# Performance work log

Hardware: AMD Instinct MI355X
Metric: run time of the kernel (lower is better)

## Reference

```python
import jax, jax.numpy as jnp
import numpy as np

N, M, E = 50000, 50000, 1600000
D_IN, HID, OUT = 128, 128, 128


def setup_inputs() -> dict:
    key = jax.random.key(0)
    ks = jax.random.split(key, 8)
    query = jax.random.normal(ks[0], (N, D_IN), jnp.float32)
    memory = jax.random.normal(ks[1], (M, D_IN), jnp.float32)
    adj_vals = jnp.ones((E,), jnp.float32)  # tf.sparse adjacency values (typically 1.0)
    Wq = jax.random.normal(ks[2], (D_IN, HID), jnp.float32) * 0.05
    bq = jnp.zeros((HID,), jnp.float32)
    Wk = jax.random.normal(ks[3], (D_IN, HID), jnp.float32) * 0.05
    bk = jnp.zeros((HID,), jnp.float32)
    Wv = jax.random.normal(ks[4], (D_IN, OUT), jnp.float32) * 0.05
    bv = jnp.zeros((OUT,), jnp.float32)
    rows = jnp.sort(jax.random.randint(ks[5], (E,), 0, N, jnp.int32))
    cols = jax.random.randint(ks[6], (E,), 0, M, jnp.int32)
    return {"query": query, "memory": memory, "adj_vals": adj_vals,
            "Wq": Wq, "bq": bq, "Wk": Wk, "bk": bk, "Wv": Wv, "bv": bv,
            "rows": rows, "cols": cols}


def reference(query, memory, adj_vals, Wq, bq, Wk, bk, Wv, bv, rows, cols):
    n = query.shape[0]
    hid = Wq.shape[1]
    # Dense projections with gelu (tfa.activations.gelu default approximate=True)
    q = jax.nn.gelu(query @ Wq + bq, approximate=True)   # [n, hid]
    k = jax.nn.gelu(memory @ Wk + bk, approximate=True)  # [m, hid]
    v = jax.nn.gelu(memory @ Wv + bv, approximate=True)  # [m, out]
    # Edge-level scores = (q_i . k_j) / sqrt(hid) * adj_val  (== coef * adj_matrix)
    scores = jnp.sum(q[rows] * k[cols], axis=-1)          # [E]
    scores = scores * (adj_vals / jnp.sqrt(jnp.float32(hid)))
    # Sparse softmax over nonzero entries of each row (tf.sparse.softmax)
    row_max = jax.ops.segment_max(scores, rows, num_segments=n, indices_are_sorted=True)
    row_max = jnp.where(jnp.isfinite(row_max), row_max, 0.0)  # rows with no edges
    e = jnp.exp(scores - row_max[rows])
    denom = jax.ops.segment_sum(e, rows, num_segments=n, indices_are_sorted=True)
    w = e / denom[rows]                                   # [E]
    # Sparse-dense matmul: out_i = sum_j w_ij * v_j
    out = jax.ops.segment_sum(w[:, None] * v[cols], rows, num_segments=n, indices_are_sorted=True)
    return out
```

## Files before the change

### kernel.cpp

```cpp
#include <hip/hip_runtime.h>
#include <hip/hip_bf16.h>
#include <hip/hip_fp8.h>
#include <math.h>

typedef _Float16 f16x4 __attribute__((ext_vector_type(4)));
typedef _Float16 f16x8 __attribute__((ext_vector_type(8)));
typedef float f32x4 __attribute__((ext_vector_type(4)));
typedef __fp16 hf8 __attribute__((ext_vector_type(8)));

#define DIM 128
#define LDST 136

#if defined(__has_builtin)
#if __has_builtin(__builtin_amdgcn_cvt_pk_fp8_f32) && __has_builtin(__builtin_amdgcn_cvt_pk_f32_fp8)
#define HAVE_FP8CVT 1
#endif
#endif

__device__ __forceinline__ unsigned int pack_fp8x4(float f0, float f1, float f2, float f3) {
#ifdef HAVE_FP8CVT
    int w = __builtin_amdgcn_cvt_pk_fp8_f32(f0, f1, 0, false);
    w = __builtin_amdgcn_cvt_pk_fp8_f32(f2, f3, w, true);
    return (unsigned int)w;
#else
    __hip_fp8_e4m3 a(f0), b(f1), c(f2), d(f3);
    return (unsigned int)a.__x | ((unsigned int)b.__x << 8) |
           ((unsigned int)c.__x << 16) | ((unsigned int)d.__x << 24);
#endif
}

__device__ __forceinline__ void dot_fp8x4(float& d, unsigned int w, const float* qv) {
#ifdef HAVE_FP8CVT
    auto lo = __builtin_amdgcn_cvt_pk_f32_fp8((int)w, false);
    auto hi = __builtin_amdgcn_cvt_pk_f32_fp8((int)w, true);
    d += lo[0] * qv[0] + lo[1] * qv[1] + hi[0] * qv[2] + hi[1] * qv[3];
#else
    for (int j = 0; j < 4; ++j) {
        __hip_fp8_e4m3 t; t.__x = (unsigned char)((w >> (8 * j)) & 0xff);
        d += (float)t * qv[j];
    }
#endif
}

__global__ __launch_bounds__(256) void prep_w_kernel(
    const float* __restrict__ Wq, const float* __restrict__ Wk,
    const float* __restrict__ Wv, _Float16* __restrict__ Wt)
{
    const float* W = (blockIdx.y == 0) ? Wq : (blockIdx.y == 1) ? Wk : Wv;
    _Float16* dst = Wt + (size_t)blockIdx.y * DIM * DIM;
    int idx = blockIdx.x * 256 + threadIdx.x;
    int k = idx >> 7;
    int n = idx & 127;
    dst[n * DIM + k] = (_Float16)W[idx];
}

__global__ __launch_bounds__(256) void row_ptr_kernel(
    const int* __restrict__ rows, int* __restrict__ row_ptr, int n, int e)
{
    int r = blockIdx.x * 256 + threadIdx.x;
    if (r > n) return;
    if (r == n) { row_ptr[n] = e; return; }
    int lo = 0, hi = e;
    while (lo < hi) {
        int mid = (lo + hi) >> 1;
        if (rows[mid] < r) lo = mid + 1; else hi = mid;
    }
    row_ptr[r] = lo;
}

__global__ __launch_bounds__(256, 2) void proj_gemm_kernel(
    const float* __restrict__ query, const float* __restrict__ memory,
    const _Float16* __restrict__ Wt,
    const float* __restrict__ bq, const float* __restrict__ bk,
    const float* __restrict__ bv,
    _Float16* __restrict__ qf, unsigned char* __restrict__ k8,
    _Float16* __restrict__ v16, int n, int m)
{
    __shared__ _Float16 xs[128 * LDST];

    int which = blockIdx.y;
    const float* X    = (which == 0) ? query : memory;
    const _Float16* Wm = Wt + (size_t)which * DIM * DIM;
    const float* bias = (which == 0) ? bq : (which == 1) ? bk : bv;
    int R             = (which == 0) ? n : m;

    int tid = threadIdx.x;
    int rowblock = blockIdx.x * 128;
    if (rowblock >= R) return;

    for (int it = 0; it < 16; ++it) {
        int flat = it * 256 + tid;
        int r  = flat >> 5;
        int c4 = (flat & 31) * 4;
        int gr = rowblock + r;
        if (gr >= R) gr = R - 1;
        float4 x = *(const float4*)(X + (size_t)gr * DIM + c4);
        f16x4 w4;
        w4[0] = (_Float16)x.x; w4[1] = (_Float16)x.y;
        w4[2] = (_Float16)x.z; w4[3] = (_Float16)x.w;
        *(f16x4*)(&xs[r * LDST + c4]) = w4;
    }
    __syncthreads();

    int wave = tid >> 6;
    int lane = tid & 63;
    int quad = lane >> 4;
    int l16  = lane & 15;
    int wrow = wave * 32;

    f16x8 afrag[2][4];
    for (int rt = 0; rt < 2; ++rt)
        for (int ks = 0; ks < 4; ++ks)
            afrag[rt][ks] = *(const f16x8*)(&xs[(wrow + rt * 16 + l16) * LDST + quad * 8 + ks * 32]);

    f32x4 acc[8][2];
    for (int ct = 0; ct < 8; ++ct) { acc[ct][0] = {0,0,0,0}; acc[ct][1] = {0,0,0,0}; }
    for (int ct = 0; ct < 8; ++ct) {
        const _Float16* wp = Wm + (size_t)(ct * 16 + l16) * DIM + quad * 8;
        for (int ks = 0; ks < 4; ++ks) {
            f16x8 b = *(const f16x8*)(wp + ks * 32);
            acc[ct][0] = __builtin_amdgcn_mfma_f32_16x16x32_f16(afrag[0][ks], b, acc[ct][0], 0, 0, 0);
            acc[ct][1] = __builtin_amdgcn_mfma_f32_16x16x32_f16(afrag[1][ks], b, acc[ct][1], 0, 0, 0);
        }
    }

    __syncthreads();
    for (int ct = 0; ct < 8; ++ct) {
        float bval = bias[ct * 16 + l16];
        for (int rt = 0; rt < 2; ++rt) {
            for (int reg = 0; reg < 4; ++reg) {
                float x = acc[ct][rt][reg] + bval;
                float t  = 0.7978845608028654f * (x + 0.044715f * x * x * x);
                float th = 1.0f - 2.0f / (__expf(2.0f * t) + 1.0f);
                float g  = 0.5f * x * (1.0f + th);
                xs[(wrow + rt * 16 + quad * 4 + reg) * LDST + ct * 16 + l16] = (_Float16)g;
            }
        }
    }
    __syncthreads();

    if (which == 1) {
        for (int it = 0; it < 8; ++it) {
            int flat = it * 256 + tid;
            int r  = flat >> 4;
            int c8 = (flat & 15) * 8;
            int gr = rowblock + r;
            if (gr < R) {
                f16x8 h = *(const f16x8*)(&xs[r * LDST + c8]);
                unsigned int w0 = pack_fp8x4((float)h[0], (float)h[1], (float)h[2], (float)h[3]);
                unsigned int w1 = pack_fp8x4((float)h[4], (float)h[5], (float)h[6], (float)h[7]);
                *(uint2*)(k8 + (size_t)gr * DIM + c8) = make_uint2(w0, w1);
            }
        }
    } else {
        _Float16* Ybase = (which == 0) ? qf : v16;
        for (int it = 0; it < 8; ++it) {
            int flat = it * 256 + tid;
            int r  = flat >> 4;
            int c8 = (flat & 15) * 8;
            int gr = rowblock + r;
            if (gr < R) {
                f16x8 vv = *(const f16x8*)(&xs[r * LDST + c8]);
                *(f16x8*)(Ybase + (size_t)gr * DIM + c8) = vv;
            }
        }
    }
}

__global__ __launch_bounds__(256) void edge_attn_kernel(
    const __fp16* __restrict__ qf, const unsigned char* __restrict__ k8,
    const __fp16* __restrict__ v16, const float* __restrict__ adj_vals,
    const int* __restrict__ cols, const int* __restrict__ row_ptr,
    float* __restrict__ out, int n)
{
    int row = blockIdx.x * 4 + (threadIdx.x >> 6);
    if (row >= n) return;
    int lane    = threadIdx.x & 63;
    int quarter = lane >> 4;
    int l16     = lane & 15;

    int start = row_ptr[row];
    int end   = row_ptr[row + 1];

    float qv[8];
    {
        hf8 q8 = *(const hf8*)(qf + (size_t)row * DIM + l16 * 8);
#pragma unroll
        for (int j = 0; j < 8; ++j) qv[j] = (float)q8[j];
    }

    float s_sum = 0.0f;
    float acc[8];
#pragma unroll
    for (int j = 0; j < 8; ++j) acc[j] = 0.0f;

    const float scale = 0.08838834764831845f;

    for (int g = start; g < end; g += 8) {
        int eA = g + quarter;
        int eB = g + 4 + quarter;
        bool vA = eA < end;
        bool vB = eB < end;
        int last = end - 1;
        int iA = vA ? eA : last;
        int iB = vB ? eB : last;
        int   cA = cols[iA];
        int   cB = cols[iB];
        float aA = adj_vals[iA] * scale;
        float aB = adj_vals[iB] * scale;

        uint2 rA = *(const uint2*)(k8 + (size_t)cA * DIM + l16 * 8);
        uint2 rB = *(const uint2*)(k8 + (size_t)cB * DIM + l16 * 8);
        hf8 vA8 = *(const hf8*)(v16 + (size_t)cA * DIM + l16 * 8);
        hf8 vB8 = *(const hf8*)(v16 + (size_t)cB * DIM + l16 * 8);

        float dA = 0.0f, dB = 0.0f;
        dot_fp8x4(dA, rA.x, qv);
        dot_fp8x4(dA, rA.y, qv + 4);
        dot_fp8x4(dB, rB.x, qv);
        dot_fp8x4(dB, rB.y, qv + 4);
        dA += __shfl_xor(dA, 1); dB += __shfl_xor(dB, 1);
        dA += __shfl_xor(dA, 2); dB += __shfl_xor(dB, 2);
        dA += __shfl_xor(dA, 4); dB += __shfl_xor(dB, 4);
        dA += __shfl_xor(dA, 8); dB += __shfl_xor(dB, 8);

        float pA_ = vA ? __expf(dA * aA) : 0.0f;
        float pB_ = vB ? __expf(dB * aB) : 0.0f;
        s_sum += pA_ + pB_;
#pragma unroll
        for (int j = 0; j < 8; ++j)
            acc[j] += pA_ * (float)vA8[j] + pB_ * (float)vB8[j];
    }

    s_sum += __shfl_xor(s_sum, 16);
    s_sum += __shfl_xor(s_sum, 32);
#pragma unroll
    for (int j = 0; j < 8; ++j) {
        acc[j] += __shfl_xor(acc[j], 16);
        acc[j] += __shfl_xor(acc[j], 32);
    }
    float inv = (s_sum > 0.0f) ? 1.0f / s_sum : 0.0f;

    if (quarter == 0) {
        float4* dst = (float4*)(out + (size_t)row * DIM + l16 * 8);
        dst[0] = make_float4(acc[0] * inv, acc[1] * inv, acc[2] * inv, acc[3] * inv);
        dst[1] = make_float4(acc[4] * inv, acc[5] * inv, acc[6] * inv, acc[7] * inv);
    }
}

extern "C" void kernel_launch(void* const* d_in, const int* in_sizes, int n_in,
                              void* d_out, int out_size, void* d_ws, size_t ws_size,
                              hipStream_t stream)
{
    const float* query    = (const float*)d_in[0];
    const float* memory   = (const float*)d_in[1];
    const float* adj_vals = (const float*)d_in[2];
    const float* Wq       = (const float*)d_in[3];
    const float* bq       = (const float*)d_in[4];
    const float* Wk       = (const float*)d_in[5];
    const float* bk       = (const float*)d_in[6];
    const float* Wv       = (const float*)d_in[7];
    const float* bv       = (const float*)d_in[8];
    const int*   rows     = (const int*)d_in[9];
    const int*   cols     = (const int*)d_in[10];
    float* out = (float*)d_out;

    int n = in_sizes[0] / DIM;
    int m = in_sizes[1] / DIM;
    int e = in_sizes[9];

    char* ws = (char*)d_ws;
    size_t off = 0;
    _Float16* Wt = (_Float16*)(ws + off); off += (size_t)3 * DIM * DIM * 2;
    _Float16* qf = (_Float16*)(ws + off); off += (size_t)n * DIM * 2;
    _Float16* v16 = (_Float16*)(ws + off); off += (size_t)m * DIM * 2;
    unsigned char* k8 = (unsigned char*)(ws + off); off += (size_t)m * DIM;
    int* row_ptr = (int*)(ws + off);      off += (size_t)(n + 1) * 4;

    prep_w_kernel<<<dim3(64, 3), 256, 0, stream>>>(Wq, Wk, Wv, Wt);

    row_ptr_kernel<<<dim3((n + 1 + 255) / 256), 256, 0, stream>>>(rows, row_ptr, n, e);

    proj_gemm_kernel<<<dim3((n + 127) / 128, 3), 256, 0, stream>>>(
        query, memory, Wt, bq, bk, bv, qf, k8, v16, n, m);

    edge_attn_kernel<<<dim3((n + 3) / 4), 256, 0, stream>>>(
        (const __fp16*)qf, k8, (const __fp16*)v16, adj_vals, cols, row_ptr, out, n);
}
```

Baseline: 236.4 us.

## Bucket edges by column range within each row and pack col/adj pairs

Adds a per-call counting sort that reorders each row's edges into 16 column buckets. Column indices and adjacency values are packed into one uint2 array, so the attention kernel does one load per edge instead of two. Edges whose columns fall in the same range are then processed closer together across rows, which should improve cache locality for the k8/v16 gathers. The cost is three extra kernels, a memset, global atomics, and an extra write and read of an E-sized buffer on every call. The attention scale is also folded into q once per row.

```diff
diff --git a/kernel.cpp b/kernel.cpp
--- a/kernel.cpp
+++ b/kernel.cpp
@@ -10,6 +10,7 @@
 
 #define DIM 128
 #define LDST 136
+#define NB 16
 
 #if defined(__has_builtin)
 #if __has_builtin(__builtin_amdgcn_cvt_pk_fp8_f32) && __has_builtin(__builtin_amdgcn_cvt_pk_f32_fp8)
@@ -66,6 +67,45 @@
         if (rows[mid] < r) lo = mid + 1; else hi = mid;
     }
     row_ptr[r] = lo;
+}
+
+__global__ __launch_bounds__(256) void count_kernel(
+    const int* __restrict__ rows, const int* __restrict__ cols,
+    int* __restrict__ cnt, int e, int bsize)
+{
+    int i = blockIdx.x * 256 + threadIdx.x;
+    if (i >= e) return;
+    int b = cols[i] / bsize;
+    atomicAdd(&cnt[rows[i] * NB + b], 1);
+}
+
+__global__ __launch_bounds__(256) void prefix_kernel(
+    const int* __restrict__ row_ptr, int* __restrict__ cnt, int n)
+{
+    int r = blockIdx.x * 256 + threadIdx.x;
+    if (r >= n) return;
+    int acc = row_ptr[r];
+    for (int b = 0; b < NB; ++b) {
+        int c = cnt[r * NB + b];
+        cnt[r * NB + b] = acc;
+        acc += c;
+    }
+}
+
+__global__ __launch_bounds__(256) void scatter_kernel(
+    const int* __restrict__ rows, const int* __restrict__ cols,
+    const float* __restrict__ adj, int* __restrict__ cnt,
+    uint2* __restrict__ packed, int e, int bsize)
+{
+    int i = blockIdx.x * 256 + threadIdx.x;
+    if (i >= e) return;
+    int c = cols[i];
+    int b = c / bsize;
+    int slot = atomicAdd(&cnt[rows[i] * NB + b], 1);
+    uint2 p;
+    p.x = (unsigned int)c;
+    p.y = __float_as_uint(adj[i]);
+    packed[slot] = p;
 }
 
 __global__ __launch_bounds__(256, 2) void proj_gemm_kernel(
@@ -169,9 +209,8 @@
 
 __global__ __launch_bounds__(256) void edge_attn_kernel(
     const __fp16* __restrict__ qf, const unsigned char* __restrict__ k8,
-    const __fp16* __restrict__ v16, const float* __restrict__ adj_vals,
-    const int* __restrict__ cols, const int* __restrict__ row_ptr,
-    float* __restrict__ out, int n)
+    const __fp16* __restrict__ v16, const uint2* __restrict__ packed,
+    const int* __restrict__ row_ptr, float* __restrict__ out, int n)
 {
     int row = blockIdx.x * 4 + (threadIdx.x >> 6);
     if (row >= n) return;
@@ -182,19 +221,18 @@
     int start = row_ptr[row];
     int end   = row_ptr[row + 1];
 
+    const float scale = 0.08838834764831845f;
     float qv[8];
     {
         hf8 q8 = *(const hf8*)(qf + (size_t)row * DIM + l16 * 8);
 #pragma unroll
-        for (int j = 0; j < 8; ++j) qv[j] = (float)q8[j];
+        for (int j = 0; j < 8; ++j) qv[j] = (float)q8[j] * scale;
     }
 
     float s_sum = 0.0f;
     float acc[8];
 #pragma unroll
     for (int j = 0; j < 8; ++j) acc[j] = 0.0f;
-
-    const float scale = 0.08838834764831845f;
 
     for (int g = start; g < end; g += 8) {
         int eA = g + quarter;
@@ -204,10 +242,12 @@
         int last = end - 1;
         int iA = vA ? eA : last;
         int iB = vB ? eB : last;
-        int   cA = cols[iA];
-        int   cB = cols[iB];
-        float aA = adj_vals[iA] * scale;
-        float aB = adj_vals[iB] * scale;
+        uint2 pkA = packed[iA];
+        uint2 pkB = packed[iB];
+        int   cA = (int)pkA.x;
+        int   cB = (int)pkB.x;
+        float aA = __uint_as_float(pkA.y);
+        float aB = __uint_as_float(pkB.y);
 
         uint2 rA = *(const uint2*)(k8 + (size_t)cA * DIM + l16 * 8);
         uint2 rB = *(const uint2*)(k8 + (size_t)cB * DIM + l16 * 8);
@@ -268,6 +308,7 @@
     int n = in_sizes[0] / DIM;
     int m = in_sizes[1] / DIM;
     int e = in_sizes[9];
+    int bsize = (m + NB - 1) / NB;
 
     char* ws = (char*)d_ws;
     size_t off = 0;
@@ -275,15 +316,23 @@
     _Float16* qf = (_Float16*)(ws + off); off += (size_t)n * DIM * 2;
     _Float16* v16 = (_Float16*)(ws + off); off += (size_t)m * DIM * 2;
     unsigned char* k8 = (unsigned char*)(ws + off); off += (size_t)m * DIM;
+    uint2* packed = (uint2*)(ws + off);   off += (size_t)e * 8;
     int* row_ptr = (int*)(ws + off);      off += (size_t)(n + 1) * 4;
+    off = (off + 15) & ~(size_t)15;
+    int* cnt = (int*)(ws + off);          off += (size_t)n * NB * 4;
 
     prep_w_kernel<<<dim3(64, 3), 256, 0, stream>>>(Wq, Wk, Wv, Wt);
 
     row_ptr_kernel<<<dim3((n + 1 + 255) / 256), 256, 0, stream>>>(rows, row_ptr, n, e);
+
+    hipMemsetAsync(cnt, 0, (size_t)n * NB * 4, stream);
+    count_kernel<<<dim3((e + 255) / 256), 256, 0, stream>>>(rows, cols, cnt, e, bsize);
+    prefix_kernel<<<dim3((n + 255) / 256), 256, 0, stream>>>(row_ptr, cnt, n);
+    scatter_kernel<<<dim3((e + 255) / 256), 256, 0, stream>>>(rows, cols, adj_vals, cnt, packed, e, bsize);
 
     proj_gemm_kernel<<<dim3((n + 127) / 128, 3), 256, 0, stream>>>(
         query, memory, Wt, bq, bk, bv, qf, k8, v16, n, m);
 
     edge_attn_kernel<<<dim3((n + 3) / 4), 256, 0, stream>>>(
-        (const __fp16*)qf, k8, (const __fp16*)v16, adj_vals, cols, row_ptr, out, n);
-}
+        (const __fp16*)qf, k8, (const __fp16*)v16, packed, row_ptr, out, n);
+}
```

Measured after the change: 304.4 us. +28.8%, slower.

## Interleave fp8 K and fp16 V into one per-node record for edge gathers

Applied to the files above, without the earlier changes.

The projection kernel now writes each memory node's fp8 key row and fp16 value row into a single 384-byte record. The separate k8 and v16 buffers are gone. Each edge gather in the attention kernel therefore reads one contiguous region instead of two distant buffers, which is meant to improve DRAM and cache locality of the random column gathers. It also folds the 1/sqrt(hid) scale into q once per row and adds nontemporal hints on the streamed cols/adj_vals loads and the output stores. The risk is that the record layout changes little if gathers are already cache-line bound, and the nontemporal hints could hurt reuse.

```diff
diff --git a/kernel.cpp b/kernel.cpp
--- a/kernel.cpp
+++ b/kernel.cpp
@@ -10,6 +10,7 @@
 
 #define DIM 128
 #define LDST 136
+#define KVREC 384
 
 #if defined(__has_builtin)
 #if __has_builtin(__builtin_amdgcn_cvt_pk_fp8_f32) && __has_builtin(__builtin_amdgcn_cvt_pk_f32_fp8)
@@ -73,8 +74,8 @@
     const _Float16* __restrict__ Wt,
     const float* __restrict__ bq, const float* __restrict__ bk,
     const float* __restrict__ bv,
-    _Float16* __restrict__ qf, unsigned char* __restrict__ k8,
-    _Float16* __restrict__ v16, int n, int m)
+    _Float16* __restrict__ qf, unsigned char* __restrict__ kvrec,
+    int n, int m)
 {
     __shared__ _Float16 xs[128 * LDST];
 
@@ -149,11 +150,10 @@
                 f16x8 h = *(const f16x8*)(&xs[r * LDST + c8]);
                 unsigned int w0 = pack_fp8x4((float)h[0], (float)h[1], (float)h[2], (float)h[3]);
                 unsigned int w1 = pack_fp8x4((float)h[4], (float)h[5], (float)h[6], (float)h[7]);
-                *(uint2*)(k8 + (size_t)gr * DIM + c8) = make_uint2(w0, w1);
+                *(uint2*)(kvrec + (size_t)gr * KVREC + c8) = make_uint2(w0, w1);
             }
         }
-    } else {
-        _Float16* Ybase = (which == 0) ? qf : v16;
+    } else if (which == 2) {
         for (int it = 0; it < 8; ++it) {
             int flat = it * 256 + tid;
             int r  = flat >> 4;
@@ -161,17 +161,27 @@
             int gr = rowblock + r;
             if (gr < R) {
                 f16x8 vv = *(const f16x8*)(&xs[r * LDST + c8]);
-                *(f16x8*)(Ybase + (size_t)gr * DIM + c8) = vv;
+                *(f16x8*)(kvrec + (size_t)gr * KVREC + 128 + c8 * 2) = vv;
             }
         }
+    } else {
+        for (int it = 0; it < 8; ++it) {
+            int flat = it * 256 + tid;
+            int r  = flat >> 4;
+            int c8 = (flat & 15) * 8;
+            int gr = rowblock + r;
+            if (gr < R) {
+                f16x8 vv = *(const f16x8*)(&xs[r * LDST + c8]);
+                *(f16x8*)(qf + (size_t)gr * DIM + c8) = vv;
+            }
+        }
     }
 }
 
 __global__ __launch_bounds__(256) void edge_attn_kernel(
-    const __fp16* __restrict__ qf, const unsigned char* __restrict__ k8,
-    const __fp16* __restrict__ v16, const float* __restrict__ adj_vals,
-    const int* __restrict__ cols, const int* __restrict__ row_ptr,
-    float* __restrict__ out, int n)
+    const __fp16* __restrict__ qf, const unsigned char* __restrict__ kvrec,
+    const float* __restrict__ adj_vals, const int* __restrict__ cols,
+    const int* __restrict__ row_ptr, float* __restrict__ out, int n)
 {
     int row = blockIdx.x * 4 + (threadIdx.x >> 6);
     if (row >= n) return;
@@ -182,19 +192,18 @@
     int start = row_ptr[row];
     int end   = row_ptr[row + 1];
 
+    const float scale = 0.08838834764831845f;
     float qv[8];
     {
-        hf8 q8 = *(const hf8*)(qf + (size_t)row * DIM + l16 * 8);
+        hf8 q8 = __builtin_nontemporal_load((const hf8*)(qf + (size_t)row * DIM + l16 * 8));
 #pragma unroll
-        for (int j = 0; j < 8; ++j) qv[j] = (float)q8[j];
+        for (int j = 0; j < 8; ++j) qv[j] = (float)q8[j] * scale;
     }
 
     float s_sum = 0.0f;
     float acc[8];
 #pragma unroll
     for (int j = 0; j < 8; ++j) acc[j] = 0.0f;
-
-    const float scale = 0.08838834764831845f;
 
     for (int g = start; g < end; g += 8) {
         int eA = g + quarter;
@@ -204,15 +213,17 @@
         int last = end - 1;
         int iA = vA ? eA : last;
         int iB = vB ? eB : last;
-        int   cA = cols[iA];
-        int   cB = cols[iB];
-        float aA = adj_vals[iA] * scale;
-        float aB = adj_vals[iB] * scale;
-
-        uint2 rA = *(const uint2*)(k8 + (size_t)cA * DIM + l16 * 8);
-        uint2 rB = *(const uint2*)(k8 + (size_t)cB * DIM + l16 * 8);
-        hf8 vA8 = *(const hf8*)(v16 + (size_t)cA * DIM + l16 * 8);
-        hf8 vB8 = *(const hf8*)(v16 + (size_t)cB * DIM + l16 * 8);
+        int   cA = __builtin_nontemporal_load(cols + iA);
+        int   cB = __builtin_nontemporal_load(cols + iB);
+        float aA = __builtin_nontemporal_load(adj_vals + iA);
+        float aB = __builtin_nontemporal_load(adj_vals + iB);
+
+        const unsigned char* rAp = kvrec + (size_t)cA * KVREC;
+        const unsigned char* rBp = kvrec + (size_t)cB * KVREC;
+        uint2 rA = *(const uint2*)(rAp + l16 * 8);
+        uint2 rB = *(const uint2*)(rBp + l16 * 8);
+        hf8 vA8 = *(const hf8*)(rAp + 128 + l16 * 16);
+        hf8 vB8 = *(const hf8*)(rBp + 128 + l16 * 16);
 
         float dA = 0.0f, dB = 0.0f;
         dot_fp8x4(dA, rA.x, qv);
@@ -242,9 +253,11 @@
     float inv = (s_sum > 0.0f) ? 1.0f / s_sum : 0.0f;
 
     if (quarter == 0) {
-        float4* dst = (float4*)(out + (size_t)row * DIM + l16 * 8);
-        dst[0] = make_float4(acc[0] * inv, acc[1] * inv, acc[2] * inv, acc[3] * inv);
-        dst[1] = make_float4(acc[4] * inv, acc[5] * inv, acc[6] * inv, acc[7] * inv);
+        float* dst = out + (size_t)row * DIM + l16 * 8;
+        f32x4 o0 = {acc[0] * inv, acc[1] * inv, acc[2] * inv, acc[3] * inv};
+        f32x4 o1 = {acc[4] * inv, acc[5] * inv, acc[6] * inv, acc[7] * inv};
+        __builtin_nontemporal_store(o0, (f32x4*)dst);
+        __builtin_nontemporal_store(o1, (f32x4*)(dst + 4));
     }
 }
 
@@ -273,8 +286,7 @@
     size_t off = 0;
     _Float16* Wt = (_Float16*)(ws + off); off += (size_t)3 * DIM * DIM * 2;
     _Float16* qf = (_Float16*)(ws + off); off += (size_t)n * DIM * 2;
-    _Float16* v16 = (_Float16*)(ws + off); off += (size_t)m * DIM * 2;
-    unsigned char* k8 = (unsigned char*)(ws + off); off += (size_t)m * DIM;
+    unsigned char* kvrec = (unsigned char*)(ws + off); off += (size_t)m * KVREC;
     int* row_ptr = (int*)(ws + off);      off += (size_t)(n + 1) * 4;
 
     prep_w_kernel<<<dim3(64, 3), 256, 0, stream>>>(Wq, Wk, Wv, Wt);
@@ -282,8 +294,8 @@
     row_ptr_kernel<<<dim3((n + 1 + 255) / 256), 256, 0, stream>>>(rows, row_ptr, n, e);
 
     proj_gemm_kernel<<<dim3((n + 127) / 128, 3), 256, 0, stream>>>(
-        query, memory, Wt, bq, bk, bv, qf, k8, v16, n, m);
+        query, memory, Wt, bq, bk, bv, qf, kvrec, n, m);
 
     edge_attn_kernel<<<dim3((n + 3) / 4), 256, 0, stream>>>(
-        (const __fp16*)qf, k8, (const __fp16*)v16, adj_vals, cols, row_ptr, out, n);
-}
+        (const __fp16*)qf, kvrec, adj_vals, cols, row_ptr, out, n);
+}
```

New measurement: 238.7 us. About the same (+1.0%).
